# Kernel optimization log

Hardware: AMD Instinct MI355X
Metric: run time of the kernel (lower is better)

## Reference

```python
import jax, jax.numpy as jnp
import numpy as np

DIM = 128
NUM_HEADS = 16
DPH = DIM // NUM_HEADS
N_ATOMS = 50000
N_EDGES = 400000
LN_EPS = 1e-5


def setup_inputs() -> dict:
    key = jax.random.key(0)
    ks = jax.random.split(key, 12)
    inp = {
        "node_feat": jax.random.normal(ks[0], (N_ATOMS, DIM), jnp.float32),
        "edge_feat": jax.random.normal(ks[1], (N_EDGES, NUM_HEADS, DPH), jnp.float32),
        "edge_vec": jax.random.normal(ks[2], (N_EDGES, 3, 1, 1), jnp.float32),
        "radial": jax.random.uniform(ks[3], (N_EDGES,), jnp.float32),
        "qkv_w": jax.random.normal(ks[4], (DIM, 3 * DIM), jnp.float32) / np.sqrt(DIM),
        "qkv_b": jnp.zeros((3 * DIM,), jnp.float32),
        "out_w": jax.random.normal(ks[5], (DIM, DIM), jnp.float32) / np.sqrt(DIM),
        "out_b": jnp.zeros((DIM,), jnp.float32),
        "ln_g": jnp.ones((DIM,), jnp.float32),
        "ln_b": jnp.zeros((DIM,), jnp.float32),
        "row": jax.random.randint(ks[6], (N_EDGES,), 0, N_ATOMS, jnp.int32),
        "col": jax.random.randint(ks[7], (N_EDGES,), 0, N_ATOMS, jnp.int32),
        "natoms": N_ATOMS,
    }
    return inp


def _layer_norm(x, g, b):
    mu = jnp.mean(x, axis=-1, keepdims=True)
    var = jnp.mean(jnp.square(x - mu), axis=-1, keepdims=True)
    return (x - mu) * jax.lax.rsqrt(var + LN_EPS) * g + b


def reference(node_feat, edge_feat, edge_vec, radial, qkv_w, qkv_b, out_w, out_b,
              ln_g, ln_b, row, col, natoms):
    # LayerNorm + QKV projection (dense)
    h = _layer_norm(node_feat, ln_g, ln_b)                     # [N, D]
    qkv = h @ qkv_w + qkv_b                                    # [N, 3D]
    qkv = qkv.reshape(-1, NUM_HEADS, 3 * DPH)                  # [N, H, 3*Dh]
    q, k, v = qkv[..., :DPH], qkv[..., DPH:2 * DPH], qkv[..., 2 * DPH:]
    # Gather by edge indices
    q_row, k_col, v_col = q[row], k[col], v[col]               # [E, H, Dh]
    # Per-edge attention (exact erf GELU, matching torch nn.GELU default)
    attn = jax.nn.gelu(jnp.sum(q_row * k_col, axis=-1), approximate=False)
    attn = attn * radial[:, None]                              # [E, H]
    # Scalar message + scatter-add
    m_feat = v_col * edge_feat * attn[..., None]               # [E, H, Dh]
    m_feat = jax.ops.segment_sum(m_feat, row, num_segments=natoms)
    m_feat = m_feat.reshape(natoms, DIM)                       # [N, D]
    # Vector message + scatter-add
    m_vec = v_col[:, None, :, :] * edge_vec                    # [E, 3, H, Dh]
    m_vec = jax.ops.segment_sum(m_vec, row, num_segments=natoms)
    delta_node_vec = m_vec.reshape(natoms, 3, DIM)             # [N, 3, D]
    delta_node_feat = m_feat @ out_w + out_b                   # [N, D]
    return delta_node_feat, delta_node_vec
```

## Files before the change

### kernel.cpp

```cpp
#include <hip/hip_runtime.h>
#include <math.h>

#define DIM 128
#define NHEADS 16
#define DPH 8
#define NATOMS 50000
#define NEDGES 400000
#define LN_EPS 1e-5f

typedef float f32x4 __attribute__((ext_vector_type(4)));
typedef short s16x8 __attribute__((ext_vector_type(8)));

static __device__ __forceinline__ unsigned short f2bf(float f) {
  unsigned u = __builtin_bit_cast(unsigned, f);
  unsigned r = (u + 0x7FFFu + ((u >> 16) & 1u)) >> 16;
  return (unsigned short)r;
}
static __device__ __forceinline__ unsigned packbf(float lo, float hi) {
  return (unsigned)f2bf(lo) | ((unsigned)f2bf(hi) << 16);
}
static __device__ __forceinline__ float bflo(unsigned u) {
  return __builtin_bit_cast(float, u << 16);
}
static __device__ __forceinline__ float bfhi(unsigned u) {
  return __builtin_bit_cast(float, u & 0xffff0000u);
}

static __device__ __forceinline__ float gelu_fast(float x) {
  const float c0 = 0.7978845608028654f;
  const float c1 = 0.044715f;
  float u = c0 * (x + c1 * x * x * x);
  return __fdividef(x, 1.0f + __expf(-2.0f * u));
}

#define HIST_NB ((NEDGES + 255) / 256)
#define SCAN_NB 196
#define LN_NB (NATOMS / 16)

__global__ __launch_bounds__(256) void k_convert(
    const float* __restrict__ qkv_w, const float* __restrict__ out_w,
    unsigned short* __restrict__ wTq, unsigned short* __restrict__ wTo,
    int* __restrict__ cnt)
{
  const int idx = blockIdx.x * 256 + threadIdx.x;
  if (idx < NATOMS) cnt[idx] = 0;
  if (idx < 384 * 128) {
    const int c = idx >> 7, k = idx & 127;
    wTq[idx] = f2bf(qkv_w[k * 384 + c]);
  } else {
    const int i2 = idx - 384 * 128;
    const int c = i2 >> 7, k = i2 & 127;
    wTo[i2] = f2bf(out_w[k * 128 + c]);
  }
}

__global__ __launch_bounds__(256) void k_ln_qkv_hist(
    const float* __restrict__ node, const unsigned short* __restrict__ wTq,
    const float* __restrict__ bias, const float* __restrict__ g,
    const float* __restrict__ beta, unsigned* __restrict__ qb,
    unsigned* __restrict__ kvb, const int* __restrict__ row,
    int* __restrict__ cnt)
{
  if (blockIdx.x >= LN_NB) {
    const int e = (blockIdx.x - LN_NB) * 256 + threadIdx.x;
    if (e < NEDGES) atomicAdd(&cnt[row[e]], 1);
    return;
  }

  __shared__ float hpad[16][132];
  __shared__ float so[16][388];
  const int a0 = blockIdx.x * 16;
  const int tid = threadIdx.x;
  const int wid = tid >> 6;
  const int lane = tid & 63;

  for (int j = 0; j < 4; ++j) {
    const int a = wid * 4 + j;
    const float x0 = node[(size_t)(a0 + a) * DIM + lane];
    const float x1 = node[(size_t)(a0 + a) * DIM + 64 + lane];
    float s = x0 + x1;
    #pragma unroll
    for (int m = 1; m < 64; m <<= 1) s += __shfl_xor(s, m);
    const float mu = s * (1.0f / 128.0f);
    const float d0 = x0 - mu, d1 = x1 - mu;
    float v = d0 * d0 + d1 * d1;
    #pragma unroll
    for (int m = 1; m < 64; m <<= 1) v += __shfl_xor(v, m);
    const float rs = rsqrtf(v * (1.0f / 128.0f) + LN_EPS);
    hpad[a][lane]      = d0 * rs * g[lane]      + beta[lane];
    hpad[a][64 + lane] = d1 * rs * g[64 + lane] + beta[64 + lane];
  }
  __syncthreads();

  const int lrow = lane & 15;
  const int lquad = lane >> 4;
  const int colbase = wid * 96;

  s16x8 afrag[4];
  #pragma unroll
  for (int ks = 0; ks < 4; ++ks) {
    const int koff = ks * 32 + lquad * 8;
    const float4 p0 = *reinterpret_cast<const float4*>(&hpad[lrow][koff]);
    const float4 p1 = *reinterpret_cast<const float4*>(&hpad[lrow][koff + 4]);
    s16x8 af;
    af[0] = (short)f2bf(p0.x); af[1] = (short)f2bf(p0.y);
    af[2] = (short)f2bf(p0.z); af[3] = (short)f2bf(p0.w);
    af[4] = (short)f2bf(p1.x); af[5] = (short)f2bf(p1.y);
    af[6] = (short)f2bf(p1.z); af[7] = (short)f2bf(p1.w);
    afrag[ks] = af;
  }

  f32x4 acc[6];
  #pragma unroll
  for (int tt = 0; tt < 6; ++tt) acc[tt] = (f32x4){0.f, 0.f, 0.f, 0.f};

  #pragma unroll
  for (int tt = 0; tt < 6; ++tt) {
    const int cg = colbase + tt * 16 + lrow;
    #pragma unroll
    for (int ks = 0; ks < 4; ++ks) {
      const s16x8 bf = *reinterpret_cast<const s16x8*>(
          &wTq[(size_t)cg * 128 + ks * 32 + lquad * 8]);
      acc[tt] = __builtin_amdgcn_mfma_f32_16x16x32_bf16(afrag[ks], bf, acc[tt], 0, 0, 0);
    }
  }

  #pragma unroll
  for (int tt = 0; tt < 6; ++tt) {
    const int cg = colbase + tt * 16 + lrow;
    const float bz = bias[cg];
    const int hj = cg / 24;
    const int off = cg - hj * 24;
    int moff;
    if (off < 8)       moff = hj * 8 + off;
    else if (off < 16) moff = 128 + (hj * 8 + off - 8) * 2;
    else               moff = 128 + (hj * 8 + off - 16) * 2 + 1;
    #pragma unroll
    for (int r = 0; r < 4; ++r)
      so[lquad * 4 + r][moff] = acc[tt][r] + bz;
  }
  __syncthreads();

  #pragma unroll
  for (int kk = 0; kk < 4; ++kk) {
    const int i = tid + kk * 256;
    const int rowi = i >> 6;
    const int c2 = i & 63;
    qb[(size_t)(a0 + rowi) * 64 + c2] =
        packbf(so[rowi][2 * c2], so[rowi][2 * c2 + 1]);
  }
  #pragma unroll
  for (int kk = 0; kk < 8; ++kk) {
    const int i = tid + kk * 256;
    const int rowi = i >> 7;
    const int c = i & 127;
    kvb[(size_t)(a0 + rowi) * 128 + c] =
        packbf(so[rowi][128 + 2 * c], so[rowi][128 + 2 * c + 1]);
  }
}

__global__ __launch_bounds__(256) void k_scan1(const int* __restrict__ cnt,
                                               int* __restrict__ locx,
                                               int* __restrict__ psum) {
  __shared__ int sh[256];
  const int tid = threadIdx.x;
  const int i = blockIdx.x * 256 + tid;
  const int v = (i < NATOMS) ? cnt[i] : 0;
  sh[tid] = v;
  __syncthreads();
  #pragma unroll
  for (int off = 1; off < 256; off <<= 1) {
    const int cur = sh[tid];
    const int add = (tid >= off) ? sh[tid - off] : 0;
    __syncthreads();
    sh[tid] = cur + add;
    __syncthreads();
  }
  if (i < NATOMS) locx[i] = sh[tid] - v;
  if (tid == 255) psum[blockIdx.x] = sh[255];
}

__global__ __launch_bounds__(256) void k_scan23(const int* __restrict__ psum,
                                                const int* __restrict__ locx,
                                                int* __restrict__ base,
                                                int* __restrict__ cursor) {
  __shared__ int ws[4];
  const int bid = blockIdx.x;
  const int tid = threadIdx.x;
  const int lane = tid & 63;
  const int wid = tid >> 6;

  int s = (tid < bid) ? psum[tid] : 0;
  #pragma unroll
  for (int m = 1; m < 64; m <<= 1) s += __shfl_xor(s, m);
  if (lane == 0) ws[wid] = s;
  __syncthreads();
  const int off = ws[0] + ws[1] + ws[2] + ws[3];

  const int i = bid * 256 + tid;
  if (i < NATOMS) {
    const int b = locx[i] + off;
    base[i] = b;
    cursor[i] = b;
  }
  if (bid == 0 && tid == 0) base[NATOMS] = NEDGES;
}

__global__ __launch_bounds__(256) void k_scatter(
    const int* __restrict__ row, const int* __restrict__ col,
    const float* __restrict__ radial, const float* __restrict__ evec,
    int* __restrict__ cursor, int4* __restrict__ descA,
    float2* __restrict__ descB)
{
  const int e = blockIdx.x * 256 + threadIdx.x;
  if (e < NEDGES) {
    const int p = atomicAdd(&cursor[row[e]], 1);
    descA[p] = make_int4(e, col[e], __float_as_int(radial[e]),
                         __float_as_int(evec[(size_t)e * 3]));
    descB[p] = make_float2(evec[(size_t)e * 3 + 1], evec[(size_t)e * 3 + 2]);
  }
}

__global__ __launch_bounds__(256) void k_edge_csr(
    const unsigned* __restrict__ qb, const uint2* __restrict__ kvb,
    const float2* __restrict__ ef2, const int4* __restrict__ descA,
    const float2* __restrict__ descB, const int* __restrict__ base,
    unsigned* __restrict__ mfeatw, float* __restrict__ outvec)
{
  const int tid = threadIdx.x;
  const int a = blockIdx.x * 4 + (tid >> 6);
  const int t = tid & 63;

  const int pBeg = __builtin_amdgcn_readfirstlane(base[a]);
  const int pEnd = __builtin_amdgcn_readfirstlane(base[a + 1]);

  float f0 = 0.f, f1 = 0.f;
  float va0 = 0.f, va1 = 0.f, vb0 = 0.f, vb1 = 0.f, vc0 = 0.f, vc1 = 0.f;

  if (pBeg < pEnd) {
    const unsigned qp = qb[(size_t)a * 64 + t];
    const float q0 = bflo(qp), q1 = bfhi(qp);
    const int pEnd_ = pEnd, pLast = pEnd - 1;

    int4 u0, u1, u2, u3;
    float2 w0, w1, w2, w3;
    uint2 kvA0, kvA1, kvA2, kvA3, kvB0, kvB1, kvB2, kvB3;
    float2 efA0, efA1, efA2, efA3, efB0, efB1, efB2, efB3;
    float rA0, rA1, rA2, rA3, xA0, xA1, xA2, xA3;
    float yA0, yA1, yA2, yA3, zA0, zA1, zA2, zA3;
    float rB0, rB1, rB2, rB3, xB0, xB1, xB2, xB3;
    float yB0, yB1, yB2, yB3, zB0, zB1, zB2, zB3;

#define LOAD_DESC(P) do {                                                   \
    const int j0_ = ((P)     <= pLast) ? (P)     : pLast;                   \
    const int j1_ = ((P) + 1 <= pLast) ? (P) + 1 : pLast;                   \
    const int j2_ = ((P) + 2 <= pLast) ? (P) + 2 : pLast;                   \
    const int j3_ = ((P) + 3 <= pLast) ? (P) + 3 : pLast;                   \
    u0 = descA[j0_]; w0 = descB[j0_];                                       \
    u1 = descA[j1_]; w1 = descB[j1_];                                       \
    u2 = descA[j2_]; w2 = descB[j2_];                                       \
    u3 = descA[j3_]; w3 = descB[j3_];                                       \
  } while (0)

#define COPY_PAY(S) do {                                                    \
    r##S##0 = __int_as_float(u0.z); x##S##0 = __int_as_float(u0.w);         \
    y##S##0 = w0.x; z##S##0 = w0.y;                                         \
    r##S##1 = __int_as_float(u1.z); x##S##1 = __int_as_float(u1.w);         \
    y##S##1 = w1.x; z##S##1 = w1.y;                                         \
    r##S##2 = __int_as_float(u2.z); x##S##2 = __int_as_float(u2.w);         \
    y##S##2 = w2.x; z##S##2 = w2.y;                                         \
    r##S##3 = __int_as_float(u3.z); x##S##3 = __int_as_float(u3.w);         \
    y##S##3 = w3.x; z##S##3 = w3.y;                                         \
  } while (0)

#define ISSUE_DATA(S) do {                                                  \
    kv##S##0 = kvb[(size_t)(unsigned)u0.y * 64 + t];                        \
    ef##S##0 = ef2[(size_t)(unsigned)u0.x * 64 + t];                        \
    kv##S##1 = kvb[(size_t)(unsigned)u1.y * 64 + t];                        \
    ef##S##1 = ef2[(size_t)(unsigned)u1.x * 64 + t];                        \
    kv##S##2 = kvb[(size_t)(unsigned)u2.y * 64 + t];                        \
    ef##S##2 = ef2[(size_t)(unsigned)u2.x * 64 + t];                        \
    kv##S##3 = kvb[(size_t)(unsigned)u3.y * 64 + t];                        \
    ef##S##3 = ef2[(size_t)(unsigned)u3.x * 64 + t];                        \
  } while (0)

#define EDGE1(KV, EF, RR, XX, YY, ZZ, MM) do {                              \
    const float kx0_ = bflo(KV.x), kx1_ = bflo(KV.y);                       \
    const float vx0_ = bfhi(KV.x) * (MM), vx1_ = bfhi(KV.y) * (MM);         \
    float pd_ = q0 * kx0_; pd_ = fmaf(q1, kx1_, pd_);                       \
    pd_ += __shfl_xor(pd_, 1); pd_ += __shfl_xor(pd_, 2);                   \
    const float at_ = gelu_fast(pd_) * (RR);                                \
    f0 = fmaf(vx0_ * EF.x, at_, f0);                                        \
    f1 = fmaf(vx1_ * EF.y, at_, f1);                                        \
    va0 = fmaf(vx0_, (XX), va0); va1 = fmaf(vx1_, (XX), va1);               \
    vb0 = fmaf(vx0_, (YY), vb0); vb1 = fmaf(vx1_, (YY), vb1);               \
    vc0 = fmaf(vx0_, (ZZ), vc0); vc1 = fmaf(vx1_, (ZZ), vc1);               \
  } while (0)

#define COMPUTE(S, P) do {                                                  \
    const float m1_ = ((P) + 1 < pEnd_) ? 1.f : 0.f;                        \
    const float m2_ = ((P) + 2 < pEnd_) ? 1.f : 0.f;                        \
    const float m3_ = ((P) + 3 < pEnd_) ? 1.f : 0.f;                        \
    EDGE1(kv##S##0, ef##S##0, r##S##0, x##S##0, y##S##0, z##S##0, 1.f);     \
    EDGE1(kv##S##1, ef##S##1, r##S##1, x##S##1, y##S##1, z##S##1, m1_);     \
    EDGE1(kv##S##2, ef##S##2, r##S##2, x##S##2, y##S##2, z##S##2, m2_);     \
    EDGE1(kv##S##3, ef##S##3, r##S##3, x##S##3, y##S##3, z##S##3, m3_);     \
  } while (0)

    LOAD_DESC(pBeg);
    COPY_PAY(A); ISSUE_DATA(A);
    LOAD_DESC(pBeg + 4);
    COPY_PAY(B); ISSUE_DATA(B);
    LOAD_DESC(pBeg + 8);

    int p = pBeg;
    while (true) {
      COMPUTE(A, p);
      p += 4; if (p >= pEnd_) break;
      COPY_PAY(A); ISSUE_DATA(A);
      LOAD_DESC(p + 8);
      COMPUTE(B, p);
      p += 4; if (p >= pEnd_) break;
      COPY_PAY(B); ISSUE_DATA(B);
      LOAD_DESC(p + 8);
    }

#undef LOAD_DESC
#undef COPY_PAY
#undef ISSUE_DATA
#undef EDGE1
#undef COMPUTE
  }

  mfeatw[(size_t)a * 64 + t] = packbf(f0, f1);
  float* ov = outvec + (size_t)a * 384 + 2 * t;
  *reinterpret_cast<float2*>(ov)       = make_float2(va0, va1);
  *reinterpret_cast<float2*>(ov + 128) = make_float2(vb0, vb1);
  *reinterpret_cast<float2*>(ov + 256) = make_float2(vc0, vc1);
}

__global__ __launch_bounds__(256) void k_out(
    const unsigned short* __restrict__ mfeatb,
    const unsigned short* __restrict__ wTo,
    const float* __restrict__ bias, float* __restrict__ out)
{
  __shared__ float so[16][132];
  const int a0 = blockIdx.x * 16;
  const int tid = threadIdx.x;
  const int wid = tid >> 6;
  const int lane = tid & 63;
  const int lrow = lane & 15;
  const int lquad = lane >> 4;

  s16x8 afrag[4];
  #pragma unroll
  for (int ks = 0; ks < 4; ++ks)
    afrag[ks] = *reinterpret_cast<const s16x8*>(
        &mfeatb[(size_t)(a0 + lrow) * 128 + ks * 32 + lquad * 8]);

  f32x4 acc[2];
  acc[0] = (f32x4){0.f, 0.f, 0.f, 0.f};
  acc[1] = (f32x4){0.f, 0.f, 0.f, 0.f};

  #pragma unroll
  for (int tt = 0; tt < 2; ++tt) {
    const int cg = wid * 32 + tt * 16 + lrow;
    #pragma unroll
    for (int ks = 0; ks < 4; ++ks) {
      const s16x8 bf = *reinterpret_cast<const s16x8*>(
          &wTo[(size_t)cg * 128 + ks * 32 + lquad * 8]);
      acc[tt] = __builtin_amdgcn_mfma_f32_16x16x32_bf16(afrag[ks], bf, acc[tt], 0, 0, 0);
    }
  }

  #pragma unroll
  for (int tt = 0; tt < 2; ++tt) {
    const int cg = wid * 32 + tt * 16 + lrow;
    const float bz = bias[cg];
    #pragma unroll
    for (int r = 0; r < 4; ++r)
      so[lquad * 4 + r][cg] = acc[tt][r] + bz;
  }
  __syncthreads();

  f32x4* out4 = (f32x4*)out;
  #pragma unroll
  for (int kk = 0; kk < 2; ++kk) {
    const int idx4 = tid + kk * 256;
    const int rowi = idx4 >> 5;
    const int c4 = idx4 & 31;
    out4[(size_t)(a0 + rowi) * 32 + c4] =
        *reinterpret_cast<const f32x4*>(&so[rowi][c4 * 4]);
  }
}

extern "C" void kernel_launch(void* const* d_in, const int* in_sizes, int n_in,
                              void* d_out, int out_size, void* d_ws, size_t ws_size,
                              hipStream_t stream) {
  const float* node_feat = (const float*)d_in[0];
  const float* edge_feat = (const float*)d_in[1];
  const float* edge_vec  = (const float*)d_in[2];
  const float* radial    = (const float*)d_in[3];
  const float* qkv_w     = (const float*)d_in[4];
  const float* qkv_b     = (const float*)d_in[5];
  const float* out_w     = (const float*)d_in[6];
  const float* out_b     = (const float*)d_in[7];
  const float* ln_g      = (const float*)d_in[8];
  const float* ln_b      = (const float*)d_in[9];
  const int*   row       = (const int*)d_in[10];
  const int*   col       = (const int*)d_in[11];

  float* out      = (float*)d_out;
  float* out_feat = out;
  float* out_vec  = out + (size_t)NATOMS * DIM;

  unsigned* qb  = (unsigned*)d_ws;
  unsigned* kvb = qb + (size_t)NATOMS * 64;
  unsigned short* mfeatb = (unsigned short*)(kvb + (size_t)NATOMS * 128);
  unsigned short* wTq = mfeatb + (size_t)NATOMS * 128;
  unsigned short* wTo = wTq + 384 * 128;
  int4* descA  = (int4*)(wTo + 128 * 128);
  float2* descB = (float2*)(descA + NEDGES);
  int* cnt    = (int*)(descB + NEDGES);
  int* base   = cnt + NATOMS;
  int* cursor = base + NATOMS + 1;
  int* locx   = cursor + NATOMS;
  int* psum   = locx + NATOMS;

  k_convert<<<256, 256, 0, stream>>>(qkv_w, out_w, wTq, wTo, cnt);

  k_ln_qkv_hist<<<LN_NB + HIST_NB, 256, 0, stream>>>(
      node_feat, wTq, qkv_b, ln_g, ln_b, qb, kvb, row, cnt);

  k_scan1<<<SCAN_NB, 256, 0, stream>>>(cnt, locx, psum);
  k_scan23<<<SCAN_NB, 256, 0, stream>>>(psum, locx, base, cursor);
  k_scatter<<<HIST_NB, 256, 0, stream>>>(row, col, radial, edge_vec, cursor,
                                         descA, descB);

  k_edge_csr<<<NATOMS / 4, 256, 0, stream>>>(
      qb, (const uint2*)kvb, (const float2*)edge_feat, descA, descB, base,
      (unsigned*)mfeatb, out_vec);

  k_out<<<NATOMS / 16, 256, 0, stream>>>(mfeatb, wTo, out_b, out_feat);
}
```

Measured before the change: 207.0 us.

## Move LN+QKV work into scatter kernel and vectorize histogram pass

The histogram now runs as its own small kernel that reads four row indices per thread with an int4 load. The LayerNorm+QKV projection blocks are moved out of the histogram launch and co-launched with the edge scatter kernel, so the dense projection overlaps the atomic scatter rather than the histogram. This puts the small histogram ahead of the scans with less work in front of it. The cost is one extra kernel launch, and a larger fused grid whose block mix is uneven.

```diff
diff --git a/kernel.cpp b/kernel.cpp
--- a/kernel.cpp
+++ b/kernel.cpp
@@ -33,11 +33,12 @@
   return __fdividef(x, 1.0f + __expf(-2.0f * u));
 }
 
-#define HIST_NB ((NEDGES + 255) / 256)
+#define HIST4_NB ((NEDGES / 4 + 255) / 256)
+#define SCAT_NB ((NEDGES + 255) / 256)
 #define SCAN_NB 196
 #define LN_NB (NATOMS / 16)
 
-__global__ __launch_bounds__(256) void k_convert(
+__global__ __launch_bounds__(256) void k_prep(
     const float* __restrict__ qkv_w, const float* __restrict__ out_w,
     unsigned short* __restrict__ wTq, unsigned short* __restrict__ wTo,
     int* __restrict__ cnt)
@@ -54,22 +55,90 @@
   }
 }
 
-__global__ __launch_bounds__(256) void k_ln_qkv_hist(
+__global__ __launch_bounds__(256) void k_hist4(const int4* __restrict__ row4,
+                                               int* __restrict__ cnt)
+{
+  const int e4 = blockIdx.x * 256 + threadIdx.x;
+  if (e4 < NEDGES / 4) {
+    const int4 r = row4[e4];
+    atomicAdd(&cnt[r.x], 1);
+    atomicAdd(&cnt[r.y], 1);
+    atomicAdd(&cnt[r.z], 1);
+    atomicAdd(&cnt[r.w], 1);
+  }
+}
+
+__global__ __launch_bounds__(256) void k_scan1(const int* __restrict__ cnt,
+                                               int* __restrict__ locx,
+                                               int* __restrict__ psum) {
+  __shared__ int sh[256];
+  const int tid = threadIdx.x;
+  const int i = blockIdx.x * 256 + tid;
+  const int v = (i < NATOMS) ? cnt[i] : 0;
+  sh[tid] = v;
+  __syncthreads();
+  #pragma unroll
+  for (int off = 1; off < 256; off <<= 1) {
+    const int cur = sh[tid];
+    const int add = (tid >= off) ? sh[tid - off] : 0;
+    __syncthreads();
+    sh[tid] = cur + add;
+    __syncthreads();
+  }
+  if (i < NATOMS) locx[i] = sh[tid] - v;
+  if (tid == 255) psum[blockIdx.x] = sh[255];
+}
+
+__global__ __launch_bounds__(256) void k_scan23(const int* __restrict__ psum,
+                                                const int* __restrict__ locx,
+                                                int* __restrict__ base,
+                                                int* __restrict__ cursor) {
+  __shared__ int ws[4];
+  const int bid = blockIdx.x;
+  const int tid = threadIdx.x;
+  const int lane = tid & 63;
+  const int wid = tid >> 6;
+
+  int s = (tid < bid) ? psum[tid] : 0;
+  #pragma unroll
+  for (int m = 1; m < 64; m <<= 1) s += __shfl_xor(s, m);
+  if (lane == 0) ws[wid] = s;
+  __syncthreads();
+  const int off = ws[0] + ws[1] + ws[2] + ws[3];
+
+  const int i = bid * 256 + tid;
+  if (i < NATOMS) {
+    const int b = locx[i] + off;
+    base[i] = b;
+    cursor[i] = b;
+  }
+  if (bid == 0 && tid == 0) base[NATOMS] = NEDGES;
+}
+
+__global__ __launch_bounds__(256) void k_scatter_ln(
+    const int* __restrict__ row, const int* __restrict__ col,
+    const float* __restrict__ radial, const float* __restrict__ evec,
+    int* __restrict__ cursor, int4* __restrict__ descA,
+    float2* __restrict__ descB,
     const float* __restrict__ node, const unsigned short* __restrict__ wTq,
     const float* __restrict__ bias, const float* __restrict__ g,
     const float* __restrict__ beta, unsigned* __restrict__ qb,
-    unsigned* __restrict__ kvb, const int* __restrict__ row,
-    int* __restrict__ cnt)
+    unsigned* __restrict__ kvb)
 {
-  if (blockIdx.x >= LN_NB) {
-    const int e = (blockIdx.x - LN_NB) * 256 + threadIdx.x;
-    if (e < NEDGES) atomicAdd(&cnt[row[e]], 1);
+  if (blockIdx.x < SCAT_NB) {
+    const int e = blockIdx.x * 256 + threadIdx.x;
+    if (e < NEDGES) {
+      const int p = atomicAdd(&cursor[row[e]], 1);
+      descA[p] = make_int4(e, col[e], __float_as_int(radial[e]),
+                           __float_as_int(evec[(size_t)e * 3]));
+      descB[p] = make_float2(evec[(size_t)e * 3 + 1], evec[(size_t)e * 3 + 2]);
+    }
     return;
   }
 
   __shared__ float hpad[16][132];
   __shared__ float so[16][388];
-  const int a0 = blockIdx.x * 16;
+  const int a0 = (blockIdx.x - SCAT_NB) * 16;
   const int tid = threadIdx.x;
   const int wid = tid >> 6;
   const int lane = tid & 63;
@@ -156,68 +225,6 @@
     const int c = i & 127;
     kvb[(size_t)(a0 + rowi) * 128 + c] =
         packbf(so[rowi][128 + 2 * c], so[rowi][128 + 2 * c + 1]);
-  }
-}
-
-__global__ __launch_bounds__(256) void k_scan1(const int* __restrict__ cnt,
-                                               int* __restrict__ locx,
-                                               int* __restrict__ psum) {
-  __shared__ int sh[256];
-  const int tid = threadIdx.x;
-  const int i = blockIdx.x * 256 + tid;
-  const int v = (i < NATOMS) ? cnt[i] : 0;
-  sh[tid] = v;
-  __syncthreads();
-  #pragma unroll
-  for (int off = 1; off < 256; off <<= 1) {
-    const int cur = sh[tid];
-    const int add = (tid >= off) ? sh[tid - off] : 0;
-    __syncthreads();
-    sh[tid] = cur + add;
-    __syncthreads();
-  }
-  if (i < NATOMS) locx[i] = sh[tid] - v;
-  if (tid == 255) psum[blockIdx.x] = sh[255];
-}
-
-__global__ __launch_bounds__(256) void k_scan23(const int* __restrict__ psum,
-                                                const int* __restrict__ locx,
-                                                int* __restrict__ base,
-                                                int* __restrict__ cursor) {
-  __shared__ int ws[4];
-  const int bid = blockIdx.x;
-  const int tid = threadIdx.x;
-  const int lane = tid & 63;
-  const int wid = tid >> 6;
-
-  int s = (tid < bid) ? psum[tid] : 0;
-  #pragma unroll
-  for (int m = 1; m < 64; m <<= 1) s += __shfl_xor(s, m);
-  if (lane == 0) ws[wid] = s;
-  __syncthreads();
-  const int off = ws[0] + ws[1] + ws[2] + ws[3];
-
-  const int i = bid * 256 + tid;
-  if (i < NATOMS) {
-    const int b = locx[i] + off;
-    base[i] = b;
-    cursor[i] = b;
-  }
-  if (bid == 0 && tid == 0) base[NATOMS] = NEDGES;
-}
-
-__global__ __launch_bounds__(256) void k_scatter(
-    const int* __restrict__ row, const int* __restrict__ col,
-    const float* __restrict__ radial, const float* __restrict__ evec,
-    int* __restrict__ cursor, int4* __restrict__ descA,
-    float2* __restrict__ descB)
-{
-  const int e = blockIdx.x * 256 + threadIdx.x;
-  if (e < NEDGES) {
-    const int p = atomicAdd(&cursor[row[e]], 1);
-    descA[p] = make_int4(e, col[e], __float_as_int(radial[e]),
-                         __float_as_int(evec[(size_t)e * 3]));
-    descB[p] = make_float2(evec[(size_t)e * 3 + 1], evec[(size_t)e * 3 + 2]);
   }
 }
 
@@ -427,15 +434,16 @@
   int* locx   = cursor + NATOMS;
   int* psum   = locx + NATOMS;
 
-  k_convert<<<256, 256, 0, stream>>>(qkv_w, out_w, wTq, wTo, cnt);
-
-  k_ln_qkv_hist<<<LN_NB + HIST_NB, 256, 0, stream>>>(
-      node_feat, wTq, qkv_b, ln_g, ln_b, qb, kvb, row, cnt);
+  k_prep<<<256, 256, 0, stream>>>(qkv_w, out_w, wTq, wTo, cnt);
+
+  k_hist4<<<HIST4_NB, 256, 0, stream>>>((const int4*)row, cnt);
 
   k_scan1<<<SCAN_NB, 256, 0, stream>>>(cnt, locx, psum);
   k_scan23<<<SCAN_NB, 256, 0, stream>>>(psum, locx, base, cursor);
-  k_scatter<<<HIST_NB, 256, 0, stream>>>(row, col, radial, edge_vec, cursor,
-                                         descA, descB);
+
+  k_scatter_ln<<<SCAT_NB + LN_NB, 256, 0, stream>>>(
+      row, col, radial, edge_vec, cursor, descA, descB,
+      node_feat, wTq, qkv_b, ln_g, ln_b, qb, kvb);
 
   k_edge_csr<<<NATOMS / 4, 256, 0, stream>>>(
       qb, (const uint2*)kvb, (const float2*)edge_feat, descA, descB, base,
```

New measurement: 199.1 us, median of 2. 1.04x faster.
